# Kernel tuning notes

Measured on AMD Instinct MI355X. Metric: run time of the kernel, lower is better.

## Reference

```python
import jax, jax.numpy as jnp
import numpy as np

# ---- static config (matches init_kwargs) ----
N0, N1 = 150000, 75000          # al nodes, test nodes
E = 200000                       # edges per edge type
D = 128                          # dim_h
L = 3                            # n_layers
T = 4                            # netypes
NAL = 50000                      # n_al vocab
NC = 3                           # n_classes
T_SRCS = [0, 0, 1, 1]
T_TGTS = [0, 1, 0, 1]
NODE_COUNTS = [N0, N1]


def setup_inputs() -> dict:
    key = jax.random.key(0)
    ks = jax.random.split(key, 16)
    x0_ids = jax.random.randint(ks[0], (N0,), 0, NAL, dtype=jnp.int32)
    x1_ids = jnp.zeros((N1,), dtype=jnp.int32)  # emb_test has a single row

    def make_edges(k, n_src, n_dst):
        k1, k2 = jax.random.split(k)
        src = jax.random.randint(k1, (E,), 0, n_src, dtype=jnp.int32)
        dst = jax.random.randint(k2, (E,), 0, n_dst, dtype=jnp.int32)
        return jnp.stack([src, dst])  # [2, E]

    es = [make_edges(ks[1 + j], NODE_COUNTS[T_SRCS[j]], NODE_COUNTS[T_TGTS[j]])
          for j in range(T)]

    s = 1.0 / np.sqrt(D)
    enc_al_w   = jax.random.normal(ks[5],  (NAL, D), jnp.float32) * s
    emb_test_w = jax.random.normal(ks[6],  (1, D),   jnp.float32) * s
    W_tgt = jax.random.normal(ks[7],  (L, T, D, D), jnp.float32) * s
    b_tgt = jax.random.normal(ks[8],  (L, T, D),    jnp.float32) * 0.01
    W_src = jax.random.normal(ks[9],  (L, T, D, D), jnp.float32) * s
    b_src = jax.random.normal(ks[10], (L, T, D),    jnp.float32) * 0.01
    emb_self = jax.random.normal(ks[11], (L, T, 2, D), jnp.float32) * s
    W_dec = jax.random.normal(ks[12], (NC, D), jnp.float32) * s
    b_dec = jax.random.normal(ks[13], (NC,),   jnp.float32) * 0.01
    return {
        "x0_ids": x0_ids, "x1_ids": x1_ids,
        "es0": es[0], "es1": es[1], "es2": es[2], "es3": es[3],
        "enc_al_w": enc_al_w, "emb_test_w": emb_test_w,
        "W_tgt": W_tgt, "b_tgt": b_tgt, "W_src": W_src, "b_src": b_src,
        "emb_self": emb_self, "W_dec": W_dec, "b_dec": b_dec,
    }


def reference(x0_ids, x1_ids, es0, es1, es2, es3,
              enc_al_w, emb_test_w, W_tgt, b_tgt, W_src, b_src,
              emb_self, W_dec, b_dec):
    ess = [es0, es1, es2, es3]
    # node-type embeddings
    xs = [enc_al_w[x0_ids], emb_test_w[x1_ids]]  # [N0,D], [N1,D]
    for i in range(L):
        out = [jnp.zeros((N0, D), xs[0].dtype), jnp.zeros((N1, D), xs[1].dtype)]
        for j in range(T):
            ts, tt = T_SRCS[j], T_TGTS[j]
            src, dst = ess[j][0], ess[j][1]
            # project node features first (same math as projecting gathered edges)
            h_src = xs[ts] @ W_src[i, j].T + b_src[i, j]   # lin_src(x_src)
            h_dst = xs[tt] @ W_tgt[i, j].T + b_tgt[i, j]   # lin_tgt(x_dst)
            self_flag = (dst == src).astype(jnp.int32)
            msg = h_dst[dst] + h_src[src] + emb_self[i, j][self_flag]  # [E,D]
            agg = jax.ops.segment_max(msg, dst, num_segments=NODE_COUNTS[tt])
            out[tt] = out[tt] + jax.nn.relu(agg)  # MPNN.forward applies relu
        xs = [jax.nn.relu(out[0]), jax.nn.relu(out[1])]
    last = xs[0] @ W_dec.T + b_dec                 # [N0, NC]
    return (last, jax.nn.softmax(last, axis=1))
```

## Files before the change

kernel.cpp:

```cpp
#include <hip/hip_runtime.h>
#include <hip/hip_bf16.h>

#define N0 150000
#define N1 75000
#define EE 200000
#define NAL 50000
#define NSEG (N0 + N1)
#define NSEG2 (2 * NSEG)
#define TOTE (4 * EE)

typedef unsigned short u16;
using s16x8 = __attribute__((ext_vector_type(8))) short;
using f32x4 = __attribute__((ext_vector_type(4))) float;
using u16x8 = __attribute__((ext_vector_type(8))) unsigned short;

__device__ __forceinline__ u16 f2b(float f) {
  unsigned int b = __float_as_uint(f);
  b += 0x7FFFu + ((b >> 16) & 1u);
  return (u16)(b >> 16);
}
__device__ __forceinline__ float b2f(u16 u) {
  return __uint_as_float(((unsigned int)u) << 16);
}

__global__ void sentinel_k(float* out, float val) {
  if (threadIdx.x == 0 && blockIdx.x == 0) out[0] = val;
}

__global__ __launch_bounds__(256) void prep_w(const float* __restrict__ Ws,
                                              const float* __restrict__ Wt,
                                              u16* __restrict__ BP) {
  int idx = blockIdx.x * 256 + threadIdx.x;
  int mk = idx & 16383;
  int slot = (idx >> 14) & 7;
  int i = idx >> 17;
  const int ssel[8] = {1, 0, 0, 1, 1, 1, 0, 0};
  const int sj[8]   = {0, 0, 2, 1, 2, 3, 1, 3};
  const float* W = ssel[slot] ? Ws : Wt;
  BP[idx] = f2b(W[(size_t)(i * 4 + sj[slot]) * 16384 + mk]);
}

__global__ __launch_bounds__(256) void embed2_k(const int* __restrict__ ids0,
                                                const int* __restrict__ ids1,
                                                const float* __restrict__ tab0,
                                                const float* __restrict__ tab1,
                                                u16* __restrict__ X0,
                                                u16* __restrict__ X1) {
  int idx = blockIdx.x * 256 + threadIdx.x;
  int v = idx >> 4;
  const int* ids; const float* tab; u16* X; unsigned vocab;
  if (v < N0) { ids = ids0; tab = tab0; X = X0; vocab = NAL; }
  else if (v < N0 + N1) { v -= N0; ids = ids1; tab = tab1; X = X1; vocab = 1; }
  else return;
  int q = (idx & 15) << 3;
  unsigned id = (unsigned)ids[v];
  if (id >= vocab) id = 0;
  const float* src = tab + (size_t)id * 128 + q;
  f32x4 x0 = *(const f32x4*)src;
  f32x4 x1 = *(const f32x4*)(src + 4);
  u16x8 o;
#pragma unroll
  for (int k = 0; k < 4; ++k) { o[k] = f2b(x0[k]); o[4 + k] = f2b(x1[k]); }
  *(u16x8*)(X + (size_t)v * 128 + q) = o;
}

__global__ __launch_bounds__(256) void count_all(const int* __restrict__ e0,
                                                 const int* __restrict__ e1,
                                                 const int* __restrict__ e2,
                                                 const int* __restrict__ e3,
                                                 int* __restrict__ cnt) {
  int i = blockIdx.x * 256 + threadIdx.x;
  if (i >= TOTE) return;
  int j = i / EE, r = i - j * EE;
  const int* es = (j == 0) ? e0 : (j == 1) ? e1 : (j == 2) ? e2 : e3;
  int dst = es[EE + r];
  int seg = (j & 1) ? N0 + dst : dst;
  atomicAdd(cnt + seg * 2 + (j >> 1), 1);
}

__global__ __launch_bounds__(512) void scan1_k(const int* __restrict__ cnt,
                                               int* __restrict__ off,
                                               int* __restrict__ part, int N) {
  __shared__ int sh[512];
  int t = threadIdx.x, i = blockIdx.x * 512 + t;
  int v = (i < N) ? cnt[i] : 0;
  sh[t] = v; __syncthreads();
  for (int s = 1; s < 512; s <<= 1) {
    int x = (t >= s) ? sh[t - s] : 0; __syncthreads();
    sh[t] += x; __syncthreads();
  }
  if (i < N) off[i] = sh[t] - v;
  if (t == 511) part[blockIdx.x] = sh[511];
}

__global__ __launch_bounds__(1024) void scan2_k(int* __restrict__ part, int n) {
  __shared__ int sh[1024];
  int t = threadIdx.x;
  int v = (t < n) ? part[t] : 0;
  sh[t] = v; __syncthreads();
  for (int s = 1; s < 1024; s <<= 1) {
    int x = (t >= s) ? sh[t - s] : 0; __syncthreads();
    sh[t] += x; __syncthreads();
  }
  if (t < n) part[t] = sh[t] - v;
}

__global__ __launch_bounds__(256) void scan3_k(int* __restrict__ off,
                                               const int* __restrict__ part, int N, int tot) {
  int i = blockIdx.x * 256 + threadIdx.x;
  if (i < N) off[i] += part[i >> 9];
  if (i == 0) off[N] = tot;
}

__global__ __launch_bounds__(256) void fill_all(const int* __restrict__ e0,
                                                const int* __restrict__ e1,
                                                const int* __restrict__ e2,
                                                const int* __restrict__ e3,
                                                const int* __restrict__ off,
                                                int* __restrict__ cur,
                                                int* __restrict__ einfo) {
  int i = blockIdx.x * 256 + threadIdx.x;
  if (i >= TOTE) return;
  int j = i / EE, r = i - j * EE;
  const int* es = (j == 0) ? e0 : (j == 1) ? e1 : (j == 2) ? e2 : e3;
  int src = es[r], dst = es[EE + r];
  int seg2 = ((j & 1) ? N0 + dst : dst) * 2 + (j >> 1);
  int pos = off[seg2] + atomicAdd(cur + seg2, 1);
  einfo[pos] = src | ((src == dst) ? (int)0x80000000 : 0);
}

__global__ __launch_bounds__(256, 5) void gemm_fused(const u16* __restrict__ A0, int M0, int nB0,
                                                     const u16* __restrict__ W0, int nw0,
                                                     u16* __restrict__ C00, u16* __restrict__ C01,
                                                     u16* __restrict__ C02, u16* __restrict__ C03,
                                                     const u16* __restrict__ A1, int M1,
                                                     const u16* __restrict__ W1,
                                                     u16* __restrict__ C10) {
  __shared__ u16 Al[64 * 128];
  __shared__ u16 Bl[64 * 128];
  const int t = threadIdx.x;
  const u16* A; const u16* W; int M, row0, nw;
  u16 *c0, *c1, *c2, *c3;
  if ((int)blockIdx.x < nB0) {
    A = A0; M = M0; row0 = blockIdx.x * 64; W = W0; nw = nw0;
    c0 = C00; c1 = C01; c2 = C02; c3 = C03;
  } else {
    A = A1; M = M1; row0 = (blockIdx.x - nB0) * 64; W = W1; nw = 1;
    c0 = C10; c1 = C10; c2 = C10; c3 = C10;
  }

#pragma unroll
  for (int u = 0; u < 4; ++u) {
    int c = u * 256 + t;
    int r = c >> 4, ch = c & 15;
    int rc = (row0 + r < M) ? (row0 + r) : (M - 1);
    int sw = ch ^ (r & 7);
    *(u16x8*)&Al[r * 128 + sw * 8] = *(const u16x8*)(A + (size_t)rc * 128 + ch * 8);
  }

  const int w = t >> 6, lane = t & 63;
  const int lr = lane & 15, g = lane >> 4;
  const int arow = (w * 16 + lr) * 128;

  u16x8 breg[4];
#pragma unroll
  for (int u = 0; u < 4; ++u) {
    int c = u * 256 + t;
    int r = c >> 4, ch = c & 15;
    breg[u] = *(const u16x8*)(W + r * 128 + ch * 8);
  }

  for (int ws = 0; ws < nw; ++ws) {
    u16* Cw = (ws == 0) ? c0 : (ws == 1) ? c1 : (ws == 2) ? c2 : c3;
#pragma unroll
    for (int h = 0; h < 2; ++h) {
      __builtin_amdgcn_sched_barrier(0);
      __builtin_amdgcn_s_barrier();
      __builtin_amdgcn_sched_barrier(0);
#pragma unroll
      for (int u = 0; u < 4; ++u) {
        int c = u * 256 + t;
        int r = c >> 4, ch = c & 15;
        int sw = ch ^ (r & 7);
        *(u16x8*)&Bl[r * 128 + sw * 8] = breg[u];
      }
      int nws = ws, nh = h + 1;
      if (nh == 2) { nh = 0; ++nws; }
      if (nws < nw) {
        const u16* Bn = W + (size_t)nws * 16384 + (size_t)nh * (64 * 128);
#pragma unroll
        for (int u = 0; u < 4; ++u) {
          int c = u * 256 + t;
          int r = c >> 4, ch = c & 15;
          breg[u] = *(const u16x8*)(Bn + r * 128 + ch * 8);
        }
      }
      asm volatile("s_waitcnt lgkmcnt(0)" ::: "memory");
      __builtin_amdgcn_sched_barrier(0);
      __builtin_amdgcn_s_barrier();
      __builtin_amdgcn_sched_barrier(0);

      f32x4 acc[4];
#pragma unroll
      for (int nf = 0; nf < 4; ++nf) acc[nf] = f32x4{0.f, 0.f, 0.f, 0.f};
#pragma unroll
      for (int ks = 0; ks < 4; ++ks) {
        int swz = ((ks * 4 + g) ^ (lr & 7)) * 8;
        s16x8 a = *(const s16x8*)&Al[arow + swz];
#pragma unroll
        for (int nf = 0; nf < 4; ++nf) {
          s16x8 b = *(const s16x8*)&Bl[(nf * 16 + lr) * 128 + swz];
          acc[nf] = __builtin_amdgcn_mfma_f32_16x16x32_bf16(a, b, acc[nf], 0, 0, 0);
        }
      }
#pragma unroll
      for (int nf = 0; nf < 4; ++nf) {
        int col = h * 64 + nf * 16 + lr;
#pragma unroll
        for (int j = 0; j < 4; ++j) {
          int orow = row0 + w * 16 + g * 4 + j;
          if (orow < M) Cw[(size_t)orow * 128 + col] = f2b(acc[nf][j]);
        }
      }
    }
  }
}

__global__ __launch_bounds__(256) void agg2_k(const int* __restrict__ off2,
                                              const int* __restrict__ einfo,
                                              int segbase,
                                              const u16* __restrict__ HSA,
                                              const u16* __restrict__ HSB,
                                              const u16* __restrict__ HD0,
                                              const u16* __restrict__ HD1,
                                              const float* __restrict__ bs0,
                                              const float* __restrict__ bt0,
                                              const float* __restrict__ bs1,
                                              const float* __restrict__ bt1,
                                              const float* __restrict__ esf0,
                                              const float* __restrict__ esf1,
                                              u16* __restrict__ Y, int N) {
  int idx = blockIdx.x * 256 + threadIdx.x;
  int d = idx >> 4;
  if (d >= N) return;
  int f8 = (idx & 15) << 3;
  int base = (segbase + d) * 2;
  int e0 = off2[base], e1 = off2[base + 1], e2 = off2[base + 2];

  float en[8], es_[8];
#pragma unroll
  for (int k = 0; k < 8; ++k) { en[k] = esf0[f8 + k]; es_[k] = esf0[128 + f8 + k]; }
  float m0[8];
#pragma unroll
  for (int k = 0; k < 8; ++k) m0[k] = -INFINITY;
  int e = e0;
  for (; e + 1 < e1; e += 2) {
    int i0 = einfo[e], i1 = einfo[e + 1];
    int s0 = i0 & 0x7fffffff, s1 = i1 & 0x7fffffff;
    u16x8 h0 = *(const u16x8*)(HSA + (size_t)s0 * 128 + f8);
    u16x8 h1 = *(const u16x8*)(HSA + (size_t)s1 * 128 + f8);
#pragma unroll
    for (int k = 0; k < 8; ++k) {
      float v0 = b2f(h0[k]) + ((i0 < 0) ? es_[k] : en[k]);
      float v1 = b2f(h1[k]) + ((i1 < 0) ? es_[k] : en[k]);
      m0[k] = fmaxf(m0[k], fmaxf(v0, v1));
    }
  }
  if (e < e1) {
    int i0 = einfo[e];
    int s0 = i0 & 0x7fffffff;
    u16x8 h0 = *(const u16x8*)(HSA + (size_t)s0 * 128 + f8);
#pragma unroll
    for (int k = 0; k < 8; ++k)
      m0[k] = fmaxf(m0[k], b2f(h0[k]) + ((i0 < 0) ? es_[k] : en[k]));
  }

#pragma unroll
  for (int k = 0; k < 8; ++k) { en[k] = esf1[f8 + k]; es_[k] = esf1[128 + f8 + k]; }
  float m1[8];
#pragma unroll
  for (int k = 0; k < 8; ++k) m1[k] = -INFINITY;
  e = e1;
  for (; e + 1 < e2; e += 2) {
    int i0 = einfo[e], i1 = einfo[e + 1];
    int s0 = i0 & 0x7fffffff, s1 = i1 & 0x7fffffff;
    u16x8 h0 = *(const u16x8*)(HSB + (size_t)s0 * 128 + f8);
    u16x8 h1 = *(const u16x8*)(HSB + (size_t)s1 * 128 + f8);
#pragma unroll
    for (int k = 0; k < 8; ++k) {
      float v0 = b2f(h0[k]) + ((i0 < 0) ? es_[k] : en[k]);
      float v1 = b2f(h1[k]) + ((i1 < 0) ? es_[k] : en[k]);
      m1[k] = fmaxf(m1[k], fmaxf(v0, v1));
    }
  }
  if (e < e2) {
    int i0 = einfo[e];
    int s0 = i0 & 0x7fffffff;
    u16x8 h0 = *(const u16x8*)(HSB + (size_t)s0 * 128 + f8);
#pragma unroll
    for (int k = 0; k < 8; ++k)
      m1[k] = fmaxf(m1[k], b2f(h0[k]) + ((i0 < 0) ? es_[k] : en[k]));
  }

  u16x8 hd0 = *(const u16x8*)(HD0 + (size_t)d * 128 + f8);
  u16x8 hd1 = *(const u16x8*)(HD1 + (size_t)d * 128 + f8);
  u16x8 o;
#pragma unroll
  for (int k = 0; k < 8; ++k) {
    float r0 = fmaxf(b2f(hd0[k]) + bs0[f8 + k] + bt0[f8 + k] + m0[k], 0.f);
    float r1 = fmaxf(b2f(hd1[k]) + bs1[f8 + k] + bt1[f8 + k] + m1[k], 0.f);
    o[k] = f2b(r0 + r1);
  }
  *(u16x8*)(Y + (size_t)d * 128 + f8) = o;
}

__global__ __launch_bounds__(256) void decoder_k(const u16* __restrict__ X,
                                                 const float* __restrict__ Wd,
                                                 const float* __restrict__ bd,
                                                 float* __restrict__ out) {
  int v = blockIdx.x * 256 + threadIdx.x;
  if (v >= N0) return;
  float a0 = bd[0], a1 = bd[1], a2 = bd[2];
  const u16* x = X + (size_t)v * 128;
#pragma unroll
  for (int k = 0; k < 128; k += 8) {
    u16x8 xv = *(const u16x8*)(x + k);
#pragma unroll
    for (int u = 0; u < 8; ++u) {
      float xf = b2f(xv[u]);
      a0 = fmaf(xf, Wd[k + u], a0);
      a1 = fmaf(xf, Wd[128 + k + u], a1);
      a2 = fmaf(xf, Wd[256 + k + u], a2);
    }
  }
  float mx = fmaxf(a0, fmaxf(a1, a2));
  float e0 = expf(a0 - mx), e1 = expf(a1 - mx), e2 = expf(a2 - mx);
  float inv = 1.f / (e0 + e1 + e2);
  size_t b = (size_t)v * 3;
  out[b + 0] = a0; out[b + 1] = a1; out[b + 2] = a2;
  size_t b2 = (size_t)N0 * 3 + b;
  out[b2 + 0] = e0 * inv; out[b2 + 1] = e1 * inv; out[b2 + 2] = e2 * inv;
}

extern "C" void kernel_launch(void* const* d_in, const int* in_sizes, int n_in,
                              void* d_out, int out_size, void* d_ws, size_t ws_size,
                              hipStream_t stream) {
  float* out = (float*)d_out;

  const int expect[15] = {N0, N1, 2 * EE, 2 * EE, 2 * EE, 2 * EE,
                          NAL * 128, 128, 196608, 1536, 196608, 1536,
                          3072, 384, 3};
  bool ok = (n_in == 15);
  if (ok) for (int i = 0; i < 15; ++i) ok = ok && (in_sizes[i] == expect[i]);
  if (!ok) { sentinel_k<<<1, 64, 0, stream>>>(out, 500.f); return; }

  const int* x0_ids = (const int*)d_in[0];
  const int* x1_ids = (const int*)d_in[1];
  const int* es0 = (const int*)d_in[2];
  const int* es1 = (const int*)d_in[3];
  const int* es2 = (const int*)d_in[4];
  const int* es3 = (const int*)d_in[5];
  const float* enc_al   = (const float*)d_in[6];
  const float* emb_test = (const float*)d_in[7];
  const float* W_tgt    = (const float*)d_in[8];
  const float* b_tgt    = (const float*)d_in[9];
  const float* W_src    = (const float*)d_in[10];
  const float* b_src    = (const float*)d_in[11];
  const float* emb_self = (const float*)d_in[12];
  const float* W_dec    = (const float*)d_in[13];
  const float* b_dec    = (const float*)d_in[14];

  char* base = (char*)d_ws;
  size_t pos = 0;
  auto alloc = [&](size_t bytes) -> void* {
    void* r = base + pos;
    pos += (bytes + 255) & ~(size_t)255;
    return r;
  };
  u16* xs0 = (u16*)alloc((size_t)N0 * 128 * 2);
  u16* xs1 = (u16*)alloc((size_t)N1 * 128 * 2);
  u16* P0  = (u16*)alloc((size_t)N0 * 128 * 2);
  u16* P1  = (u16*)alloc((size_t)N0 * 128 * 2);
  u16* P2  = (u16*)alloc((size_t)N0 * 128 * 2);
  u16* P3  = (u16*)alloc((size_t)N1 * 128 * 2);
  u16* P4  = (u16*)alloc((size_t)N0 * 128 * 2);
  u16* BP  = (u16*)alloc((size_t)3 * 8 * 16384 * 2);
  int* off2   = (int*)alloc((size_t)(NSEG2 + 1) * 4);
  int* einfo  = (int*)alloc((size_t)TOTE * 4);
  int* counts = (int*)alloc((size_t)NSEG2 * 4);
  int* cursor = counts;
  int* part   = (int*)alloc(1024 * 4);
  if (pos > ws_size) { sentinel_k<<<1, 64, 0, stream>>>(out, 900.f); return; }

  prep_w<<<1536, 256, 0, stream>>>(W_src, W_tgt, BP);
  embed2_k<<<((N0 + N1) * 16 + 255) / 256, 256, 0, stream>>>(x0_ids, x1_ids, enc_al, emb_test, xs0, xs1);

  const int EG = (TOTE + 255) / 256;
  const int nb = (NSEG2 + 511) / 512;
  hipMemsetAsync(counts, 0, (size_t)NSEG2 * 4, stream);
  count_all<<<EG, 256, 0, stream>>>(es0, es1, es2, es3, counts);
  scan1_k<<<nb, 512, 0, stream>>>(counts, off2, part, NSEG2);
  scan2_k<<<1, 1024, 0, stream>>>(part, nb);
  scan3_k<<<(NSEG2 + 255) / 256, 256, 0, stream>>>(off2, part, NSEG2, TOTE);
  hipMemsetAsync(cursor, 0, (size_t)NSEG2 * 4, stream);
  fill_all<<<EG, 256, 0, stream>>>(es0, es1, es2, es3, off2, cursor, einfo);

  const int G0 = (N0 + 63) / 64, G1 = (N1 + 63) / 64;
  const int GA0 = (N0 * 16 + 255) / 256, GA1 = (N1 * 16 + 255) / 256;
  for (int i = 0; i < 3; ++i) {
    const u16* BPi = BP + (size_t)i * 8 * 16384;
    gemm_fused<<<G0 + G1, 256, 0, stream>>>(xs0, N0, G0, BPi + 0 * 16384, (i < 2) ? 4 : 3,
                                            P0, P1, P2, P4,
                                            xs1, N1, BPi + 4 * 16384, P3);
    agg2_k<<<GA0, 256, 0, stream>>>(off2, einfo, 0, P0, P3, P1, P2,
                                    b_src + (size_t)(i * 4 + 0) * 128, b_tgt + (size_t)(i * 4 + 0) * 128,
                                    b_src + (size_t)(i * 4 + 2) * 128, b_tgt + (size_t)(i * 4 + 2) * 128,
                                    emb_self + (size_t)(i * 4 + 0) * 256,
                                    emb_self + (size_t)(i * 4 + 2) * 256, xs0, N0);
    if (i < 2) {
      gemm_fused<<<G1, 256, 0, stream>>>(xs1, N1, G1, BPi + 5 * 16384, 3,
                                         P3, P1, P2, P2,
                                         xs1, N1, BPi + 4 * 16384, P3);
      agg2_k<<<GA1, 256, 0, stream>>>(off2, einfo, N0, P4, P3, P1, P2,
                                      b_src + (size_t)(i * 4 + 1) * 128, b_tgt + (size_t)(i * 4 + 1) * 128,
                                      b_src + (size_t)(i * 4 + 3) * 128, b_tgt + (size_t)(i * 4 + 3) * 128,
                                      emb_self + (size_t)(i * 4 + 1) * 256,
                                      emb_self + (size_t)(i * 4 + 3) * 256, xs1, N1);
    }
  }

  decoder_k<<<(N0 + 255) / 256, 256, 0, stream>>>(xs0, W_dec, b_dec, out);
}
```

Before: 475.2 us.

## Fuse decoder into last aggregation, unroll gathers by four, reshuffle GEMM weight slots

The decoder and softmax now run inside the final layer's aggregation kernel, using a 16-lane shuffle reduction, so the separate decoder pass and the write and reread of xs0 are gone. The edge-gather loops are unrolled by four to keep more independent loads in flight. The weight slot layout is reordered so the first GEMM computes an extra projection of xs1 into a new buffer P5, and the second GEMM computes one fewer output. This adds a buffer and more registers in the aggregation kernel.

After: 513.2 us. 1.08x slower.

```diff
diff --git a/kernel.cpp b/kernel.cpp
--- a/kernel.cpp
+++ b/kernel.cpp
@@ -34,8 +34,8 @@
   int mk = idx & 16383;
   int slot = (idx >> 14) & 7;
   int i = idx >> 17;
-  const int ssel[8] = {1, 0, 0, 1, 1, 1, 0, 0};
-  const int sj[8]   = {0, 0, 2, 1, 2, 3, 1, 3};
+  const int ssel[8] = {1, 0, 0, 1, 1, 0, 1, 0};
+  const int sj[8]   = {0, 0, 2, 1, 2, 1, 3, 3};
   const float* W = ssel[slot] ? Ws : Wt;
   BP[idx] = f2b(W[(size_t)(i * 4 + sj[slot]) * 16384 + mk]);
 }
@@ -134,8 +134,8 @@
                                                      u16* __restrict__ C00, u16* __restrict__ C01,
                                                      u16* __restrict__ C02, u16* __restrict__ C03,
                                                      const u16* __restrict__ A1, int M1,
-                                                     const u16* __restrict__ W1,
-                                                     u16* __restrict__ C10) {
+                                                     const u16* __restrict__ W1, int nw1,
+                                                     u16* __restrict__ C10, u16* __restrict__ C11) {
   __shared__ u16 Al[64 * 128];
   __shared__ u16 Bl[64 * 128];
   const int t = threadIdx.x;
@@ -145,8 +145,8 @@
     A = A0; M = M0; row0 = blockIdx.x * 64; W = W0; nw = nw0;
     c0 = C00; c1 = C01; c2 = C02; c3 = C03;
   } else {
-    A = A1; M = M1; row0 = (blockIdx.x - nB0) * 64; W = W1; nw = 1;
-    c0 = C10; c1 = C10; c2 = C10; c3 = C10;
+    A = A1; M = M1; row0 = (blockIdx.x - nB0) * 64; W = W1; nw = nw1;
+    c0 = C10; c1 = C11; c2 = C11; c3 = C11;
   }
 
 #pragma unroll
@@ -239,7 +239,10 @@
                                               const float* __restrict__ bt1,
                                               const float* __restrict__ esf0,
                                               const float* __restrict__ esf1,
-                                              u16* __restrict__ Y, int N) {
+                                              u16* __restrict__ Y, int N,
+                                              const float* __restrict__ Wd,
+                                              const float* __restrict__ bd,
+                                              float* __restrict__ outp, int dec) {
   int idx = blockIdx.x * 256 + threadIdx.x;
   int d = idx >> 4;
   if (d >= N) return;
@@ -254,11 +257,25 @@
 #pragma unroll
   for (int k = 0; k < 8; ++k) m0[k] = -INFINITY;
   int e = e0;
+  for (; e + 3 < e1; e += 4) {
+    int i0 = einfo[e], i1 = einfo[e + 1], i2 = einfo[e + 2], i3 = einfo[e + 3];
+    u16x8 h0 = *(const u16x8*)(HSA + (size_t)(i0 & 0x7fffffff) * 128 + f8);
+    u16x8 h1 = *(const u16x8*)(HSA + (size_t)(i1 & 0x7fffffff) * 128 + f8);
+    u16x8 h2 = *(const u16x8*)(HSA + (size_t)(i2 & 0x7fffffff) * 128 + f8);
+    u16x8 h3 = *(const u16x8*)(HSA + (size_t)(i3 & 0x7fffffff) * 128 + f8);
+#pragma unroll
+    for (int k = 0; k < 8; ++k) {
+      float v0 = b2f(h0[k]) + ((i0 < 0) ? es_[k] : en[k]);
+      float v1 = b2f(h1[k]) + ((i1 < 0) ? es_[k] : en[k]);
+      float v2 = b2f(h2[k]) + ((i2 < 0) ? es_[k] : en[k]);
+      float v3 = b2f(h3[k]) + ((i3 < 0) ? es_[k] : en[k]);
+      m0[k] = fmaxf(m0[k], fmaxf(fmaxf(v0, v1), fmaxf(v2, v3)));
+    }
+  }
   for (; e + 1 < e1; e += 2) {
     int i0 = einfo[e], i1 = einfo[e + 1];
-    int s0 = i0 & 0x7fffffff, s1 = i1 & 0x7fffffff;
-    u16x8 h0 = *(const u16x8*)(HSA + (size_t)s0 * 128 + f8);
-    u16x8 h1 = *(const u16x8*)(HSA + (size_t)s1 * 128 + f8);
+    u16x8 h0 = *(const u16x8*)(HSA + (size_t)(i0 & 0x7fffffff) * 128 + f8);
+    u16x8 h1 = *(const u16x8*)(HSA + (size_t)(i1 & 0x7fffffff) * 128 + f8);
 #pragma unroll
     for (int k = 0; k < 8; ++k) {
       float v0 = b2f(h0[k]) + ((i0 < 0) ? es_[k] : en[k]);
@@ -268,8 +285,7 @@
   }
   if (e < e1) {
     int i0 = einfo[e];
-    int s0 = i0 & 0x7fffffff;
-    u16x8 h0 = *(const u16x8*)(HSA + (size_t)s0 * 128 + f8);
+    u16x8 h0 = *(const u16x8*)(HSA + (size_t)(i0 & 0x7fffffff) * 128 + f8);
 #pragma unroll
     for (int k = 0; k < 8; ++k)
       m0[k] = fmaxf(m0[k], b2f(h0[k]) + ((i0 < 0) ? es_[k] : en[k]));
@@ -281,11 +297,25 @@
 #pragma unroll
   for (int k = 0; k < 8; ++k) m1[k] = -INFINITY;
   e = e1;
+  for (; e + 3 < e2; e += 4) {
+    int i0 = einfo[e], i1 = einfo[e + 1], i2 = einfo[e + 2], i3 = einfo[e + 3];
+    u16x8 h0 = *(const u16x8*)(HSB + (size_t)(i0 & 0x7fffffff) * 128 + f8);
+    u16x8 h1 = *(const u16x8*)(HSB + (size_t)(i1 & 0x7fffffff) * 128 + f8);
+    u16x8 h2 = *(const u16x8*)(HSB + (size_t)(i2 & 0x7fffffff) * 128 + f8);
+    u16x8 h3 = *(const u16x8*)(HSB + (size_t)(i3 & 0x7fffffff) * 128 + f8);
+#pragma unroll
+    for (int k = 0; k < 8; ++k) {
+      float v0 = b2f(h0[k]) + ((i0 < 0) ? es_[k] : en[k]);
+      float v1 = b2f(h1[k]) + ((i1 < 0) ? es_[k] : en[k]);
+      float v2 = b2f(h2[k]) + ((i2 < 0) ? es_[k] : en[k]);
+      float v3 = b2f(h3[k]) + ((i3 < 0) ? es_[k] : en[k]);
+      m1[k] = fmaxf(m1[k], fmaxf(fmaxf(v0, v1), fmaxf(v2, v3)));
+    }
+  }
   for (; e + 1 < e2; e += 2) {
     int i0 = einfo[e], i1 = einfo[e + 1];
-    int s0 = i0 & 0x7fffffff, s1 = i1 & 0x7fffffff;
-    u16x8 h0 = *(const u16x8*)(HSB + (size_t)s0 * 128 + f8);
-    u16x8 h1 = *(const u16x8*)(HSB + (size_t)s1 * 128 + f8);
+    u16x8 h0 = *(const u16x8*)(HSB + (size_t)(i0 & 0x7fffffff) * 128 + f8);
+    u16x8 h1 = *(const u16x8*)(HSB + (size_t)(i1 & 0x7fffffff) * 128 + f8);
 #pragma unroll
     for (int k = 0; k < 8; ++k) {
       float v0 = b2f(h0[k]) + ((i0 < 0) ? es_[k] : en[k]);
@@ -295,8 +325,7 @@
   }
   if (e < e2) {
     int i0 = einfo[e];
-    int s0 = i0 & 0x7fffffff;
-    u16x8 h0 = *(const u16x8*)(HSB + (size_t)s0 * 128 + f8);
+    u16x8 h0 = *(const u16x8*)(HSB + (size_t)(i0 & 0x7fffffff) * 128 + f8);
 #pragma unroll
     for (int k = 0; k < 8; ++k)
       m1[k] = fmaxf(m1[k], b2f(h0[k]) + ((i0 < 0) ? es_[k] : en[k]));
@@ -311,35 +340,36 @@
     float r1 = fmaxf(b2f(hd1[k]) + bs1[f8 + k] + bt1[f8 + k] + m1[k], 0.f);
     o[k] = f2b(r0 + r1);
   }
-  *(u16x8*)(Y + (size_t)d * 128 + f8) = o;
-}
-
-__global__ __launch_bounds__(256) void decoder_k(const u16* __restrict__ X,
-                                                 const float* __restrict__ Wd,
-                                                 const float* __restrict__ bd,
-                                                 float* __restrict__ out) {
-  int v = blockIdx.x * 256 + threadIdx.x;
-  if (v >= N0) return;
-  float a0 = bd[0], a1 = bd[1], a2 = bd[2];
-  const u16* x = X + (size_t)v * 128;
-#pragma unroll
-  for (int k = 0; k < 128; k += 8) {
-    u16x8 xv = *(const u16x8*)(x + k);
-#pragma unroll
-    for (int u = 0; u < 8; ++u) {
-      float xf = b2f(xv[u]);
-      a0 = fmaf(xf, Wd[k + u], a0);
-      a1 = fmaf(xf, Wd[128 + k + u], a1);
-      a2 = fmaf(xf, Wd[256 + k + u], a2);
-    }
-  }
-  float mx = fmaxf(a0, fmaxf(a1, a2));
-  float e0 = expf(a0 - mx), e1 = expf(a1 - mx), e2 = expf(a2 - mx);
-  float inv = 1.f / (e0 + e1 + e2);
-  size_t b = (size_t)v * 3;
-  out[b + 0] = a0; out[b + 1] = a1; out[b + 2] = a2;
-  size_t b2 = (size_t)N0 * 3 + b;
-  out[b2 + 0] = e0 * inv; out[b2 + 1] = e1 * inv; out[b2 + 2] = e2 * inv;
+
+  if (!dec) {
+    *(u16x8*)(Y + (size_t)d * 128 + f8) = o;
+    return;
+  }
+
+  float p0 = 0.f, p1 = 0.f, p2 = 0.f;
+#pragma unroll
+  for (int k = 0; k < 8; ++k) {
+    float xf = b2f(o[k]);
+    p0 = fmaf(xf, Wd[f8 + k], p0);
+    p1 = fmaf(xf, Wd[128 + f8 + k], p1);
+    p2 = fmaf(xf, Wd[256 + f8 + k], p2);
+  }
+#pragma unroll
+  for (int m = 1; m < 16; m <<= 1) {
+    p0 += __shfl_xor(p0, m, 64);
+    p1 += __shfl_xor(p1, m, 64);
+    p2 += __shfl_xor(p2, m, 64);
+  }
+  if ((threadIdx.x & 15) == 0) {
+    float a0 = p0 + bd[0], a1 = p1 + bd[1], a2 = p2 + bd[2];
+    float mx = fmaxf(a0, fmaxf(a1, a2));
+    float x0 = expf(a0 - mx), x1 = expf(a1 - mx), x2 = expf(a2 - mx);
+    float inv = 1.f / (x0 + x1 + x2);
+    size_t b = (size_t)d * 3;
+    outp[b + 0] = a0; outp[b + 1] = a1; outp[b + 2] = a2;
+    size_t b2 = (size_t)N0 * 3 + b;
+    outp[b2 + 0] = x0 * inv; outp[b2 + 1] = x1 * inv; outp[b2 + 2] = x2 * inv;
+  }
 }
 
 extern "C" void kernel_launch(void* const* d_in, const int* in_sizes, int n_in,
@@ -384,6 +414,7 @@
   u16* P2  = (u16*)alloc((size_t)N0 * 128 * 2);
   u16* P3  = (u16*)alloc((size_t)N1 * 128 * 2);
   u16* P4  = (u16*)alloc((size_t)N0 * 128 * 2);
+  u16* P5  = (u16*)alloc((size_t)N1 * 128 * 2);
   u16* BP  = (u16*)alloc((size_t)3 * 8 * 16384 * 2);
   int* off2   = (int*)alloc((size_t)(NSEG2 + 1) * 4);
   int* einfo  = (int*)alloc((size_t)TOTE * 4);
@@ -411,23 +442,23 @@
     const u16* BPi = BP + (size_t)i * 8 * 16384;
     gemm_fused<<<G0 + G1, 256, 0, stream>>>(xs0, N0, G0, BPi + 0 * 16384, (i < 2) ? 4 : 3,
                                             P0, P1, P2, P4,
-                                            xs1, N1, BPi + 4 * 16384, P3);
+                                            xs1, N1, BPi + 4 * 16384, (i < 2) ? 2 : 1, P3, P5);
     agg2_k<<<GA0, 256, 0, stream>>>(off2, einfo, 0, P0, P3, P1, P2,
                                     b_src + (size_t)(i * 4 + 0) * 128, b_tgt + (size_t)(i * 4 + 0) * 128,
                                     b_src + (size_t)(i * 4 + 2) * 128, b_tgt + (size_t)(i * 4 + 2) * 128,
                                     emb_self + (size_t)(i * 4 + 0) * 256,
-                                    emb_self + (size_t)(i * 4 + 2) * 256, xs0, N0);
+                                    emb_self + (size_t)(i * 4 + 2) * 256, xs0, N0,
+                                    W_dec, b_dec, out, (i == 2) ? 1 : 0);
     if (i < 2) {
-      gemm_fused<<<G1, 256, 0, stream>>>(xs1, N1, G1, BPi + 5 * 16384, 3,
-                                         P3, P1, P2, P2,
-                                         xs1, N1, BPi + 4 * 16384, P3);
-      agg2_k<<<GA1, 256, 0, stream>>>(off2, einfo, N0, P4, P3, P1, P2,
+      gemm_fused<<<G1, 256, 0, stream>>>(xs1, N1, G1, BPi + 6 * 16384, 2,
+                                         P3, P2, P2, P2,
+                                         xs1, N1, BPi + 4 * 16384, 1, P3, P5);
+      agg2_k<<<GA1, 256, 0, stream>>>(off2, einfo, N0, P4, P3, P5, P2,
                                       b_src + (size_t)(i * 4 + 1) * 128, b_tgt + (size_t)(i * 4 + 1) * 128,
                                       b_src + (size_t)(i * 4 + 3) * 128, b_tgt + (size_t)(i * 4 + 3) * 128,
                                       emb_self + (size_t)(i * 4 + 1) * 256,
-                                      emb_self + (size_t)(i * 4 + 3) * 256, xs1, N1);
-    }
-  }
-
-  decoder_k<<<(N0 + 255) / 256, 256, 0, stream>>>(xs0, W_dec, b_dec, out);
-}
+                                      emb_self + (size_t)(i * 4 + 3) * 256, xs1, N1,
+                                      W_dec, b_dec, out, 0);
+    }
+  }
+}
```
